# Optimization experiments

Measured on AMD Instinct MI355X. Metric: run time of the kernel, lower is better.

Reference implementation:

```python
import jax, jax.numpy as jnp
import numpy as np

N = 16777216  # sequence length
C = 2         # binary BUY/SELL classes


def setup_inputs() -> dict:
    key = jax.random.key(0)
    k1, k2 = jax.random.split(key)
    inputs = jax.random.normal(k1, (N, C), dtype=jnp.float32)
    labels = jax.random.randint(k2, (N,), 0, 2, dtype=jnp.int64)
    return {"inputs": inputs, "labels": labels}


def _trend_segment_weights(labels):
    """weights[i] = remaining length (inclusive) until end of current run of equal labels.

    next_change[i] = next_change[i+1] + 1 if labels[i]==labels[i+1] else 0, next_change[-1]=0.
    Vectorized as a reversed running count of consecutive Trues, implemented via
    cummax of the last reset index (O(N), no sequential Python loop).
    """
    n = labels.shape[0]
    # e[i] = True iff labels[i] == labels[i+1]; e[n-1] = False
    e = jnp.concatenate([labels[:-1] == labels[1:], jnp.zeros((1,), dtype=bool)])
    f = e[::-1]
    r = jnp.arange(n, dtype=jnp.int32)
    # index of most recent False at or before position j
    last_false = jax.lax.cummax(jnp.where(f, jnp.int32(-1), r))
    count = r - last_false            # run length of Trues ending at j (0 if f[j] False)
    next_change = count[::-1]
    return (next_change + 1).astype(jnp.float32)


def reference(inputs, labels):
    # per-element cross entropy with logits (N, 2)
    logp = jax.nn.log_softmax(inputs, axis=-1)                      # (N, 2)
    ce = -jnp.take_along_axis(logp, labels[:, None], axis=-1)[:, 0]  # (N,)
    weights = _trend_segment_weights(labels)                         # (N,)
    return jnp.mean(ce * weights)
```

## Files before the change

kernel.cpp:

```cpp
#include <hip/hip_runtime.h>

#define N_ELEM 16777216
#define K 8
#define BLOCK 256
#define TILE (BLOCK * K)
#define NBLK (N_ELEM / TILE)
#define INV_N (1.0 / (double)N_ELEM)

__global__ __launch_bounds__(BLOCK, 8) void k1_all(
        const float4* __restrict__ in4, const int4* __restrict__ lab4,
        const int* __restrict__ labs, float* __restrict__ out) {
    __shared__ unsigned metaS[BLOCK];
    __shared__ double wsum[BLOCK / 64];
    const int tid = threadIdx.x;
    const long long ch = (long long)blockIdx.x * BLOCK + tid;

    float4 x[4];
    int4   lv[2];
    const float4* ip = in4 + ch * 4;
    const int4*   lp = lab4 + ch * 2;
    #pragma unroll
    for (int j = 0; j < 4; ++j) x[j] = ip[j];
    #pragma unroll
    for (int j = 0; j < 2; ++j) lv[j] = lp[j];

    float acc = 0.f, tce = 0.f, cf = 0.f;
    int prevLab = 0, lastLab = 0, firstLab = 0;
    #pragma unroll
    for (int i = K - 1; i >= 0; --i) {
        float a = (i & 1) ? x[i >> 1].z : x[i >> 1].x;
        float b = (i & 1) ? x[i >> 1].w : x[i >> 1].y;
        int m = i & 3, l;
        { int4 q = lv[i >> 2];
          l = (m == 0) ? q.x : (m == 1) ? q.y : (m == 2) ? q.z : q.w; }
        float d = l ? (a - b) : (b - a);
        float ce = __logf(1.0f + __expf(d));
        if (i == K - 1) { cf = 1.f; lastLab = l; }
        else            cf = (l == prevLab) ? cf + 1.f : 1.f;
        acc = fmaf(ce, cf, acc);
        if (cf == (float)(K - i)) tce += ce;
        prevLab = l;
        firstLab = l;
    }
    metaS[tid] = (unsigned)cf | ((unsigned)firstLab << 6) | ((unsigned)lastLab << 7);
    __syncthreads();

    long long ext = 0;
    {
        int prevLast = lastLab;
        int t = tid + 1;
        bool open = true;
        while (t < BLOCK) {
            unsigned mb = metaS[t];
            if ((int)((mb >> 6) & 1) != prevLast) { open = false; break; }
            int hb = (int)(mb & 63);
            ext += hb;
            if (hb < K) { open = false; break; }
            prevLast = (int)((mb >> 7) & 1);
            ++t;
        }
        if (open) {
            long long g = (long long)(blockIdx.x + 1) * TILE;
            while (g < N_ELEM && labs[g] == prevLast) { ++ext; ++g; }
        }
    }
    double accd = (double)acc + (double)tce * (double)ext;

    for (int o = 32; o; o >>= 1) accd += __shfl_down(accd, o);
    int wid = tid >> 6, lane = tid & 63;
    if (lane == 0) wsum[wid] = accd;
    __syncthreads();
    if (tid == 0) {
        double s = 0.0;
        for (int w = 0; w < BLOCK / 64; ++w) s += wsum[w];
        atomicAdd(out, (float)(s * INV_N));
    }
}

extern "C" void kernel_launch(void* const* d_in, const int* in_sizes, int n_in,
                              void* d_out, int out_size, void* d_ws, size_t ws_size,
                              hipStream_t stream) {
    const float* inputs = (const float*)d_in[0];
    const int* labels = (const int*)d_in[1];
    float* out = (float*)d_out;

    hipMemsetAsync(out, 0, sizeof(float), stream);
    k1_all<<<NBLK, BLOCK, 0, stream>>>(
        (const float4*)inputs, (const int4*)labels, labels, out);
}
```

Measured before the change: 277.0 us.

## Double per-thread work and compute run weights with forward prefix sums

Each thread now handles 16 elements instead of 8, with launch bounds relaxed to match, and twice the loads are issued before any compute. The per-element weight logic moves from a backward running count to a forward scan that keeps per-run sums S0 and S1 and closes each run with a closed-form weighted sum. The intent is to cut block count and cross-thread scan overhead and get more memory parallelism per thread. The cost is higher register pressure and possible loss of occupancy.

```diff
diff --git a/kernel.cpp b/kernel.cpp
--- a/kernel.cpp
+++ b/kernel.cpp
@@ -1,13 +1,13 @@
 #include <hip/hip_runtime.h>
 
 #define N_ELEM 16777216
-#define K 8
+#define K 16
 #define BLOCK 256
 #define TILE (BLOCK * K)
 #define NBLK (N_ELEM / TILE)
 #define INV_N (1.0 / (double)N_ELEM)
 
-__global__ __launch_bounds__(BLOCK, 8) void k1_all(
+__global__ __launch_bounds__(BLOCK, 4) void k1_all(
         const float4* __restrict__ in4, const int4* __restrict__ lab4,
         const int* __restrict__ labs, float* __restrict__ out) {
     __shared__ unsigned metaS[BLOCK];
@@ -15,34 +15,44 @@
     const int tid = threadIdx.x;
     const long long ch = (long long)blockIdx.x * BLOCK + tid;
 
-    float4 x[4];
-    int4   lv[2];
-    const float4* ip = in4 + ch * 4;
-    const int4*   lp = lab4 + ch * 2;
+    float4 x[8];
+    int4   lv[4];
+    const float4* ip = in4 + ch * 8;
+    const int4*   lp = lab4 + ch * 4;
     #pragma unroll
-    for (int j = 0; j < 4; ++j) x[j] = ip[j];
+    for (int j = 0; j < 8; ++j) x[j] = ip[j];
     #pragma unroll
-    for (int j = 0; j < 2; ++j) lv[j] = lp[j];
+    for (int j = 0; j < 4; ++j) lv[j] = lp[j];
+    asm volatile("" ::: "memory");
 
-    float acc = 0.f, tce = 0.f, cf = 0.f;
-    int prevLab = 0, lastLab = 0, firstLab = 0;
+    float acc = 0.f, S0 = 0.f, S1 = 0.f, runStartF = 0.f;
+    int prev = 0, firstLab = 0, h = K;
     #pragma unroll
-    for (int i = K - 1; i >= 0; --i) {
+    for (int i = 0; i < K; ++i) {
         float a = (i & 1) ? x[i >> 1].z : x[i >> 1].x;
         float b = (i & 1) ? x[i >> 1].w : x[i >> 1].y;
         int m = i & 3, l;
         { int4 q = lv[i >> 2];
           l = (m == 0) ? q.x : (m == 1) ? q.y : (m == 2) ? q.z : q.w; }
-        float d = l ? (a - b) : (b - a);
+        float t = b - a;
+        float d = l ? -t : t;
         float ce = __logf(1.0f + __expf(d));
-        if (i == K - 1) { cf = 1.f; lastLab = l; }
-        else            cf = (l == prevLab) ? cf + 1.f : 1.f;
-        acc = fmaf(ce, cf, acc);
-        if (cf == (float)(K - i)) tce += ce;
-        prevLab = l;
-        firstLab = l;
+        if (i == 0) { firstLab = l; prev = l; }
+        else if (l != prev) {
+            float L = (float)i - runStartF;
+            acc = fmaf(L, S0, acc) - S1;
+            if (h == K) h = i;
+            S0 = 0.f; S1 = 0.f; runStartF = (float)i;
+            prev = l;
+        }
+        S0 += ce;
+        S1 = fmaf(ce, (float)i - runStartF, S1);
     }
-    metaS[tid] = (unsigned)cf | ((unsigned)firstLab << 6) | ((unsigned)lastLab << 7);
+    const int lastLab = prev;
+    const float tce = S0;
+    acc = fmaf((float)K - runStartF, S0, acc) - S1;
+
+    metaS[tid] = (unsigned)h | ((unsigned)firstLab << 6) | ((unsigned)lastLab << 7);
     __syncthreads();
 
     long long ext = 0;
```

New measurement: 241.8 us. -12.7%, faster.

## Compute run-length weights with wave ballots over strided segments and two-stage reduction

Applied to the files above, without the earlier changes.

Each wave now streams 32 segments of 64 consecutive elements, one element per lane. Run boundaries come from ballot and find-first-set, and open runs are carried across segments as a pending sum, which replaces per-thread serial chunks and the shared-memory scan over 256 threads. Loads are software-prefetched one segment ahead. The float atomic and memset are replaced by per-block partials in workspace plus a single-block final kernel. The cost is narrower float2/int loads instead of float4/int4, a loop carried dependency, and an extra kernel launch.

```diff
diff --git a/kernel.cpp b/kernel.cpp
--- a/kernel.cpp
+++ b/kernel.cpp
@@ -1,80 +1,120 @@
 #include <hip/hip_runtime.h>
 
 #define N_ELEM 16777216
-#define K 8
 #define BLOCK 256
-#define TILE (BLOCK * K)
-#define NBLK (N_ELEM / TILE)
+#define WPB 4
+#define SEGS 32
+#define SPAN (SEGS * 64)
+#define BSPAN (WPB * SPAN)
+#define NBLK (N_ELEM / BSPAN)
 #define INV_N (1.0 / (double)N_ELEM)
 
-__global__ __launch_bounds__(BLOCK, 8) void k1_all(
-        const float4* __restrict__ in4, const int4* __restrict__ lab4,
-        const int* __restrict__ labs, float* __restrict__ out) {
-    __shared__ unsigned metaS[BLOCK];
-    __shared__ double wsum[BLOCK / 64];
-    const int tid = threadIdx.x;
-    const long long ch = (long long)blockIdx.x * BLOCK + tid;
+__global__ __launch_bounds__(BLOCK) void k1_partial(
+        const float2* __restrict__ in2, const int* __restrict__ labs,
+        double* __restrict__ bsum) {
+    __shared__ unsigned metaW[WPB];
+    __shared__ double wtot[WPB];
+    const int tid  = threadIdx.x;
+    const int lane = tid & 63;
+    const int w    = tid >> 6;
+    const long long spanBase = (long long)blockIdx.x * BSPAN + (long long)w * SPAN;
 
-    float4 x[4];
-    int4   lv[2];
-    const float4* ip = in4 + ch * 4;
-    const int4*   lp = lab4 + ch * 2;
-    #pragma unroll
-    for (int j = 0; j < 4; ++j) x[j] = ip[j];
-    #pragma unroll
-    for (int j = 0; j < 2; ++j) lv[j] = lp[j];
+    float acc = 0.f, pend = 0.f;
+    unsigned headLen = SPAN;
+    int seen = 0;
+    const float fopen = (float)(64 - lane);
 
-    float acc = 0.f, tce = 0.f, cf = 0.f;
-    int prevLab = 0, lastLab = 0, firstLab = 0;
-    #pragma unroll
-    for (int i = K - 1; i >= 0; --i) {
-        float a = (i & 1) ? x[i >> 1].z : x[i >> 1].x;
-        float b = (i & 1) ? x[i >> 1].w : x[i >> 1].y;
-        int m = i & 3, l;
-        { int4 q = lv[i >> 2];
-          l = (m == 0) ? q.x : (m == 1) ? q.y : (m == 2) ? q.z : q.w; }
-        float d = l ? (a - b) : (b - a);
+    long long idx0 = spanBase + lane;
+    float2 x  = in2[idx0];
+    int   lab = labs[idx0];
+    long long b0 = spanBase + 64;
+    int  blab = labs[b0 < N_ELEM ? b0 : (N_ELEM - 1)];
+
+    int firstLab = 0;
+
+    #pragma unroll 1
+    for (int s = 0; s < SEGS; ++s) {
+        float2 xn; int labn = 0, blabn = 0;
+        if (s + 1 < SEGS) {
+            long long idn = spanBase + (long long)(s + 1) * 64 + lane;
+            xn   = in2[idn];
+            labn = labs[idn];
+            long long bn = spanBase + (long long)(s + 2) * 64;
+            blabn = labs[bn < N_ELEM ? bn : (N_ELEM - 1)];
+        }
+        if (s == 0) firstLab = __shfl(lab, 0);
+
+        float t = x.y - x.x;
+        float d = lab ? -t : t;
         float ce = __logf(1.0f + __expf(d));
-        if (i == K - 1) { cf = 1.f; lastLab = l; }
-        else            cf = (l == prevLab) ? cf + 1.f : 1.f;
-        acc = fmaf(ce, cf, acc);
-        if (cf == (float)(K - i)) tce += ce;
-        prevLab = l;
-        firstLab = l;
+
+        int nl = __shfl_down(lab, 1);
+        long long bidx = spanBase + (long long)(s + 1) * 64;
+        if (lane == 63) nl = (bidx < N_ELEM) ? blab : (lab ^ 1);
+
+        unsigned long long Bm = __ballot(lab != nl);
+        unsigned long long sh = Bm >> lane;
+        int   closed = (sh != 0ull);
+        int   dist   = __ffsll(sh) - 1;
+        float wloc   = closed ? (float)(dist + 1) : fopen;
+        acc = fmaf(ce, wloc, acc);
+
+        int h = Bm ? __ffsll(Bm) : 64;
+        acc  = fmaf(pend, (float)h, acc);
+        pend = (Bm ? 0.f : pend) + (closed ? 0.f : ce);
+
+        if (!seen && Bm) { headLen = (unsigned)(s * 64 + h); seen = 1; }
+
+        if (s + 1 < SEGS) { x = xn; lab = labn; blab = blabn; }
     }
-    metaS[tid] = (unsigned)cf | ((unsigned)firstLab << 6) | ((unsigned)lastLab << 7);
+    const int lastLab = __shfl(lab, 63);
+
+    for (int o = 32; o; o >>= 1) {
+        acc  += __shfl_down(acc,  o);
+        pend += __shfl_down(pend, o);
+    }
+    if (lane == 0)
+        metaW[w] = headLen | ((unsigned)firstLab << 12) | ((unsigned)lastLab << 13);
     __syncthreads();
 
-    long long ext = 0;
-    {
-        int prevLast = lastLab;
-        int t = tid + 1;
-        bool open = true;
-        while (t < BLOCK) {
-            unsigned mb = metaS[t];
-            if ((int)((mb >> 6) & 1) != prevLast) { open = false; break; }
-            int hb = (int)(mb & 63);
-            ext += hb;
-            if (hb < K) { open = false; break; }
-            prevLast = (int)((mb >> 7) & 1);
-            ++t;
+    if (lane == 0) {
+        long long ext = 0;
+        if (pend != 0.f) {
+            int prevLast = lastLab;
+            int t2 = w + 1;
+            bool open = true;
+            while (t2 < WPB) {
+                unsigned mb = metaW[t2];
+                if ((int)((mb >> 12) & 1) != prevLast) { open = false; break; }
+                unsigned hl = mb & 0xFFFu;
+                ext += hl;
+                if (hl < SPAN) { open = false; break; }
+                prevLast = (int)((mb >> 13) & 1);
+                ++t2;
+            }
+            if (open) {
+                long long g = (long long)blockIdx.x * BSPAN + (long long)t2 * SPAN;
+                while (g < N_ELEM && labs[g] == prevLast) { ++ext; ++g; }
+            }
         }
-        if (open) {
-            long long g = (long long)(blockIdx.x + 1) * TILE;
-            while (g < N_ELEM && labs[g] == prevLast) { ++ext; ++g; }
-        }
+        wtot[w] = (double)acc + (double)pend * (double)ext;
     }
-    double accd = (double)acc + (double)tce * (double)ext;
+    __syncthreads();
+    if (tid == 0)
+        bsum[blockIdx.x] = wtot[0] + wtot[1] + wtot[2] + wtot[3];
+}
 
-    for (int o = 32; o; o >>= 1) accd += __shfl_down(accd, o);
-    int wid = tid >> 6, lane = tid & 63;
-    if (lane == 0) wsum[wid] = accd;
+__global__ __launch_bounds__(BLOCK) void k2_final(
+        const double* __restrict__ bsum, float* __restrict__ out) {
+    double s = 0.0;
+    for (int i = threadIdx.x; i < NBLK; i += BLOCK) s += bsum[i];
+    for (int o = 32; o; o >>= 1) s += __shfl_down(s, o);
+    __shared__ double wsum[BLOCK / 64];
+    int wv = threadIdx.x >> 6, lane = threadIdx.x & 63;
+    if (lane == 0) wsum[wv] = s;
     __syncthreads();
-    if (tid == 0) {
-        double s = 0.0;
-        for (int w = 0; w < BLOCK / 64; ++w) s += wsum[w];
-        atomicAdd(out, (float)(s * INV_N));
-    }
+    if (threadIdx.x == 0)
+        out[0] = (float)((wsum[0] + wsum[1] + wsum[2] + wsum[3]) * INV_N);
 }
 
 extern "C" void kernel_launch(void* const* d_in, const int* in_sizes, int n_in,
@@ -82,9 +122,9 @@
                               hipStream_t stream) {
     const float* inputs = (const float*)d_in[0];
     const int* labels = (const int*)d_in[1];
-    float* out = (float*)d_out;
+    double* bsum = (double*)d_ws;
 
-    hipMemsetAsync(out, 0, sizeof(float), stream);
-    k1_all<<<NBLK, BLOCK, 0, stream>>>(
-        (const float4*)inputs, (const int4*)labels, labels, out);
+    k1_partial<<<NBLK, BLOCK, 0, stream>>>(
+        (const float2*)inputs, labels, bsum);
+    k2_final<<<1, BLOCK, 0, stream>>>(bsum, (float*)d_out);
 }
```

Measured after the change: 233.4 us. -15.7%, faster.
